# Optimization experiments

Measured on AMD Instinct MI355X. Metric: run time of the kernel, lower is better.

Reference implementation:

```python
import jax, jax.numpy as jnp
import numpy as np

B, C, N, K, OUT = 8, 128, 8192, 16, 128

def setup_inputs() -> dict:
    key = jax.random.key(0)
    k1, k2, k3, k4 = jax.random.split(key, 4)
    x = jax.random.normal(k1, (B, C, N), dtype=jnp.float32)
    idx = jax.random.randint(k2, (B * N * K,), 0, B * N, dtype=jnp.int64)
    W = jax.random.normal(k3, (OUT, C, 1), dtype=jnp.float32) * 0.05
    b = jax.random.normal(k4, (OUT,), dtype=jnp.float32) * 0.05
    return {"x": x, "idx": idx, "W": W, "b": b}

def reference(x, idx, W, b):
    Bs, Cs, Ns = x.shape
    k = idx.shape[0] // (Bs * Ns)
    # (B,C,N) -> (B*N, C) matching torch permute(0,2,1).reshape(-1,C)
    x_flat = jnp.transpose(x, (0, 2, 1)).reshape(-1, Cs)
    # gather k neighbors per point, then max over neighbor dim
    neighbors = x_flat[idx].reshape(Bs, Ns, k, Cs)  # (B,N,k,C)
    agg = neighbors.max(axis=2)                      # (B,N,C)
    # 1x1 conv == per-point linear: (B,N,C) x (O,C) -> (B,O,N)
    out = jnp.einsum('bnc,oc->bon', agg, W[:, :, 0]) + b[None, :, None]
    return jax.nn.relu(out)
```

## Files before the change

### kernel.cpp

```cpp
#include <hip/hip_runtime.h>
#include <stdint.h>

#define B_  8
#define C_  128
#define N_  8192
#define K_  16
#define O_  128

typedef __attribute__((ext_vector_type(8))) short short8;
typedef __attribute__((ext_vector_type(4))) float f32x4;

__device__ __forceinline__ unsigned short f2bf(float f) {
    union { float f; uint32_t u; } v; v.f = f;
    uint32_t u = v.u;
    return (unsigned short)((u + 0x7FFFu + ((u >> 16) & 1u)) >> 16);
}

__device__ __forceinline__ uint32_t fwdmap(uint32_t u) {
    uint32_t s  = u & 0x80008000u;
    uint32_t xm = s - (s >> 15) + 0x80008000u;
    return u ^ xm;
}
__device__ __forceinline__ uint32_t invmap(uint32_t v) {
    uint32_t s  = (~v) & 0x80008000u;
    uint32_t xm = s - (s >> 15) + 0x80008000u;
    return v ^ xm;
}
__device__ __forceinline__ uint32_t pkmax(uint32_t a, uint32_t b) {
    uint32_t d;
    asm("v_pk_max_u16 %0, %1, %2" : "=v"(d) : "v"(a), "v"(b));
    return d;
}
__device__ __forceinline__ uint4 pkmax4(uint4 a, uint4 b) {
    return make_uint4(pkmax(a.x, b.x), pkmax(a.y, b.y),
                      pkmax(a.z, b.z), pkmax(a.w, b.w));
}

__global__ __launch_bounds__(256) void k_transpose(const float* __restrict__ x,
                                                   unsigned short* __restrict__ xt) {
    __shared__ uint32_t lds[64 * 65];
    int t    = threadIdx.x;
    int lane = t & 63;
    int wv   = t >> 6;
    int blk  = blockIdx.x;
    int b    = blk >> 7;
    int n0   = (blk & 127) * 64;

    const float* xb = x + (size_t)b * C_ * N_ + n0 + lane;
    #pragma unroll
    for (int j = 0; j < 16; ++j) {
        int c2 = wv * 16 + j;
        float f0 = xb[(size_t)(2 * c2) * N_];
        float f1 = xb[(size_t)(2 * c2 + 1) * N_];
        uint32_t pk = (uint32_t)f2bf(f0) | ((uint32_t)f2bf(f1) << 16);
        lds[c2 * 65 + lane] = fwdmap(pk);
    }
    __syncthreads();

    int rl = lane >> 4;
    int ch = lane & 15;
    #pragma unroll
    for (int it = 0; it < 4; ++it) {
        int r = it * 16 + wv * 4 + rl;
        uint32_t u0 = lds[(ch * 4 + 0) * 65 + r];
        uint32_t u1 = lds[(ch * 4 + 1) * 65 + r];
        uint32_t u2 = lds[(ch * 4 + 2) * 65 + r];
        uint32_t u3 = lds[(ch * 4 + 3) * 65 + r];
        *(uint4*)(xt + ((size_t)(b * N_ + n0 + r)) * C_ + ch * 8) =
            make_uint4(u0, u1, u2, u3);
    }
}

__global__ __launch_bounds__(256, 4) void k_main(const unsigned short* __restrict__ xt,
                                                 const int* __restrict__ idx,
                                                 const float* __restrict__ Wp,
                                                 const float* __restrict__ bp,
                                                 float* __restrict__ out) {
    __shared__ __align__(16) unsigned short agg[64 * 136];
    __shared__ int idxs[64 * K_];

    int t    = threadIdx.x;
    int lane = t & 63;
    int wv   = t >> 6;
    int blk  = blockIdx.x;
    int b    = blk >> 7;
    int n0   = (blk & 127) * 64;
    size_t pbase = (size_t)b * N_ + n0;

    const int* ip = idx + pbase * K_;
    #pragma unroll
    for (int i = 0; i < 4; ++i) idxs[t + i * 256] = ip[t + i * 256];
    __syncthreads();

    int pt  = lane >> 4;
    int cch = lane & 15;
    #pragma unroll
    for (int i = 0; i < 4; ++i) {
        int p = wv * 16 + i * 4 + pt;
        const int* qq = &idxs[p * K_];
        uint4 d[16];
        #pragma unroll
        for (int k = 0; k < 16; ++k)
            d[k] = *(const uint4*)(xt + (size_t)qq[k] * C_ + cch * 8);
        #pragma unroll
        for (int s = 8; s >= 1; s >>= 1)
            #pragma unroll
            for (int k = 0; k < s; ++k)
                d[k] = pkmax4(d[k], d[k + s]);
        uint4 v = make_uint4(invmap(d[0].x), invmap(d[0].y),
                             invmap(d[0].z), invmap(d[0].w));
        *(uint4*)&agg[p * 136 + cch * 8] = v;
    }
    __syncthreads();

    int r16 = lane & 15;
    int h   = lane >> 4;
    int wo  = wv * 32;

    short8 af[2][4];
    #pragma unroll
    for (int ot2 = 0; ot2 < 2; ++ot2)
        #pragma unroll
        for (int kk = 0; kk < 4; ++kk) {
            const float* wr = Wp + (size_t)(wo + ot2 * 16 + r16) * C_ + kk * 32 + h * 8;
            float4 a0 = *(const float4*)wr;
            float4 a1 = *(const float4*)(wr + 4);
            short8 s;
            s[0] = (short)f2bf(a0.x); s[1] = (short)f2bf(a0.y);
            s[2] = (short)f2bf(a0.z); s[3] = (short)f2bf(a0.w);
            s[4] = (short)f2bf(a1.x); s[5] = (short)f2bf(a1.y);
            s[6] = (short)f2bf(a1.z); s[7] = (short)f2bf(a1.w);
            af[ot2][kk] = s;
        }
    float4 bb[2];
    bb[0] = *(const float4*)(bp + wo + h * 4);
    bb[1] = *(const float4*)(bp + wo + 16 + h * 4);

    const size_t ob = (size_t)b * O_ * N_ + n0;
    #pragma unroll
    for (int pt4 = 0; pt4 < 4; ++pt4) {
        short8 bfr[4];
        #pragma unroll
        for (int kk = 0; kk < 4; ++kk)
            bfr[kk] = *(const short8*)&agg[(pt4 * 16 + r16) * 136 + kk * 32 + h * 8];
        #pragma unroll
        for (int ot2 = 0; ot2 < 2; ++ot2) {
            f32x4 acc = {0.f, 0.f, 0.f, 0.f};
            #pragma unroll
            for (int kk = 0; kk < 4; ++kk)
                acc = __builtin_amdgcn_mfma_f32_16x16x32_bf16(af[ot2][kk], bfr[kk], acc, 0, 0, 0);
            int orow = wo + ot2 * 16 + h * 4;
            float* op = out + ob + (size_t)orow * N_ + pt4 * 16 + r16;
            float4 bv = bb[ot2];
            op[0]              = fmaxf(acc[0] + bv.x, 0.f);
            op[(size_t)N_]     = fmaxf(acc[1] + bv.y, 0.f);
            op[(size_t)2 * N_] = fmaxf(acc[2] + bv.z, 0.f);
            op[(size_t)3 * N_] = fmaxf(acc[3] + bv.w, 0.f);
        }
    }
}

extern "C" void kernel_launch(void* const* d_in, const int* in_sizes, int n_in,
                              void* d_out, int out_size, void* d_ws, size_t ws_size,
                              hipStream_t stream) {
    const float* x    = (const float*)d_in[0];
    const int*   idx  = (const int*)d_in[1];
    const float* W    = (const float*)d_in[2];
    const float* bias = (const float*)d_in[3];
    float* out = (float*)d_out;
    unsigned short* xt = (unsigned short*)d_ws;

    hipLaunchKernelGGL(k_transpose, dim3(1024), dim3(256), 0, stream, x, xt);
    hipLaunchKernelGGL(k_main,      dim3(1024), dim3(256), 0, stream, xt, idx, W, bias, out);
}
```

Measured before the change: 52.90 us.

## Split bf16 feature table into channel planes and halve gather tile size

The transposed bf16 feature table is now stored as four 32-channel planes instead of one 128-channel row per point. The gather-max kernel reads each plane with 8-byte loads and runs two 8-way max trees per plane. The main kernel now handles 32 points per block across 2048 blocks with a higher occupancy bound. A spare block in the transpose kernel pre-converts W to bf16 when the workspace is large enough. The aim is better cache locality for the random gathers and more parallelism, at the cost of smaller, less coalesced gather segments and more blocks.

```diff
diff --git a/kernel.cpp b/kernel.cpp
--- a/kernel.cpp
+++ b/kernel.cpp
@@ -6,6 +6,8 @@
 #define N_  8192
 #define K_  16
 #define O_  128
+#define TP  32
+#define PL  ((size_t)65536 * 32)
 
 typedef __attribute__((ext_vector_type(8))) short short8;
 typedef __attribute__((ext_vector_type(4))) float f32x4;
@@ -15,7 +17,6 @@
     uint32_t u = v.u;
     return (unsigned short)((u + 0x7FFFu + ((u >> 16) & 1u)) >> 16);
 }
-
 __device__ __forceinline__ uint32_t fwdmap(uint32_t u) {
     uint32_t s  = u & 0x80008000u;
     uint32_t xm = s - (s >> 15) + 0x80008000u;
@@ -31,18 +32,36 @@
     asm("v_pk_max_u16 %0, %1, %2" : "=v"(d) : "v"(a), "v"(b));
     return d;
 }
-__device__ __forceinline__ uint4 pkmax4(uint4 a, uint4 b) {
-    return make_uint4(pkmax(a.x, b.x), pkmax(a.y, b.y),
-                      pkmax(a.z, b.z), pkmax(a.w, b.w));
-}
-
+__device__ __forceinline__ uint2 pkmax2(uint2 a, uint2 b) {
+    return make_uint2(pkmax(a.x, b.x), pkmax(a.y, b.y));
+}
+__device__ __forceinline__ uint2 tree8(const uint2 d[8]) {
+    uint2 t0 = pkmax2(d[0], d[4]), t1 = pkmax2(d[1], d[5]);
+    uint2 t2 = pkmax2(d[2], d[6]), t3 = pkmax2(d[3], d[7]);
+    t0 = pkmax2(t0, t2); t1 = pkmax2(t1, t3);
+    return pkmax2(t0, t1);
+}
+
+template<bool PREW>
 __global__ __launch_bounds__(256) void k_transpose(const float* __restrict__ x,
-                                                   unsigned short* __restrict__ xt) {
-    __shared__ uint32_t lds[64 * 65];
+                                                   unsigned short* __restrict__ xt,
+                                                   const float* __restrict__ Wp,
+                                                   unsigned short* __restrict__ Wbf) {
+    int blk = blockIdx.x;
+    if (PREW && blk == 1024) {
+        int t = threadIdx.x;
+        #pragma unroll
+        for (int i = 0; i < 32; ++i) {
+            int e = t + i * 256;
+            float2 w2 = ((const float2*)Wp)[e];
+            ((uint32_t*)Wbf)[e] = (uint32_t)f2bf(w2.x) | ((uint32_t)f2bf(w2.y) << 16);
+        }
+        return;
+    }
+    __shared__ uint32_t lds[64 * 66];
     int t    = threadIdx.x;
     int lane = t & 63;
     int wv   = t >> 6;
-    int blk  = blockIdx.x;
     int b    = blk >> 7;
     int n0   = (blk & 127) * 64;
 
@@ -53,105 +72,109 @@
         float f0 = xb[(size_t)(2 * c2) * N_];
         float f1 = xb[(size_t)(2 * c2 + 1) * N_];
         uint32_t pk = (uint32_t)f2bf(f0) | ((uint32_t)f2bf(f1) << 16);
-        lds[c2 * 65 + lane] = fwdmap(pk);
+        lds[c2 * 66 + lane] = fwdmap(pk);
     }
     __syncthreads();
 
-    int rl = lane >> 4;
-    int ch = lane & 15;
-    #pragma unroll
-    for (int it = 0; it < 4; ++it) {
-        int r = it * 16 + wv * 4 + rl;
-        uint32_t u0 = lds[(ch * 4 + 0) * 65 + r];
-        uint32_t u1 = lds[(ch * 4 + 1) * 65 + r];
-        uint32_t u2 = lds[(ch * 4 + 2) * 65 + r];
-        uint32_t u3 = lds[(ch * 4 + 3) * 65 + r];
-        *(uint4*)(xt + ((size_t)(b * N_ + n0 + r)) * C_ + ch * 8) =
+    int rr = lane >> 2;
+    int ch = lane & 3;
+    size_t rowb = (size_t)(b * N_ + n0);
+    #pragma unroll
+    for (int pl = 0; pl < 4; ++pl) {
+        int r = wv * 16 + rr;
+        uint32_t u0 = lds[(pl * 16 + ch * 4 + 0) * 66 + r];
+        uint32_t u1 = lds[(pl * 16 + ch * 4 + 1) * 66 + r];
+        uint32_t u2 = lds[(pl * 16 + ch * 4 + 2) * 66 + r];
+        uint32_t u3 = lds[(pl * 16 + ch * 4 + 3) * 66 + r];
+        *(uint4*)(xt + (size_t)pl * PL + (rowb + r) * 32 + ch * 8) =
             make_uint4(u0, u1, u2, u3);
     }
 }
 
-__global__ __launch_bounds__(256, 4) void k_main(const unsigned short* __restrict__ xt,
+template<bool PREW>
+__global__ __launch_bounds__(256, 8) void k_main(const unsigned short* __restrict__ xt,
                                                  const int* __restrict__ idx,
                                                  const float* __restrict__ Wp,
+                                                 const unsigned short* __restrict__ Wbf,
                                                  const float* __restrict__ bp,
                                                  float* __restrict__ out) {
-    __shared__ __align__(16) unsigned short agg[64 * 136];
-    __shared__ int idxs[64 * K_];
+    __shared__ __align__(16) unsigned short agg[TP * 136];
+    __shared__ int idxs[TP * K_];
 
     int t    = threadIdx.x;
     int lane = t & 63;
     int wv   = t >> 6;
     int blk  = blockIdx.x;
-    int b    = blk >> 7;
-    int n0   = (blk & 127) * 64;
+    int b    = blk >> 8;
+    int n0   = (blk & 255) * TP;
     size_t pbase = (size_t)b * N_ + n0;
 
     const int* ip = idx + pbase * K_;
-    #pragma unroll
-    for (int i = 0; i < 4; ++i) idxs[t + i * 256] = ip[t + i * 256];
+    idxs[t]       = ip[t];
+    idxs[t + 256] = ip[t + 256];
     __syncthreads();
 
-    int pt  = lane >> 4;
-    int cch = lane & 15;
-    #pragma unroll
-    for (int i = 0; i < 4; ++i) {
-        int p = wv * 16 + i * 4 + pt;
-        const int* qq = &idxs[p * K_];
-        uint4 d[16];
-        #pragma unroll
-        for (int k = 0; k < 16; ++k)
-            d[k] = *(const uint4*)(xt + (size_t)qq[k] * C_ + cch * 8);
-        #pragma unroll
-        for (int s = 8; s >= 1; s >>= 1)
-            #pragma unroll
-            for (int k = 0; k < s; ++k)
-                d[k] = pkmax4(d[k], d[k + s]);
-        uint4 v = make_uint4(invmap(d[0].x), invmap(d[0].y),
-                             invmap(d[0].z), invmap(d[0].w));
-        *(uint4*)&agg[p * 136 + cch * 8] = v;
+    int pt  = lane >> 3;
+    int cch = lane & 7;
+    int p   = wv * 8 + pt;
+    const int* qq = &idxs[p * K_];
+    #pragma unroll
+    for (int pl = 0; pl < 4; ++pl) {
+        const unsigned short* base = xt + (size_t)pl * PL + cch * 4;
+        uint2 d[8];
+        #pragma unroll
+        for (int k = 0; k < 8; ++k)
+            d[k] = *(const uint2*)(base + (size_t)qq[k] * 32);
+        uint2 r0 = tree8(d);
+        #pragma unroll
+        for (int k = 0; k < 8; ++k)
+            d[k] = *(const uint2*)(base + (size_t)qq[k + 8] * 32);
+        uint2 r1 = tree8(d);
+        uint2 r  = pkmax2(r0, r1);
+        *(uint2*)&agg[p * 136 + pl * 32 + cch * 4] =
+            make_uint2(invmap(r.x), invmap(r.y));
     }
     __syncthreads();
 
     int r16 = lane & 15;
     int h   = lane >> 4;
     int wo  = wv * 32;
-
-    short8 af[2][4];
-    #pragma unroll
-    for (int ot2 = 0; ot2 < 2; ++ot2)
-        #pragma unroll
-        for (int kk = 0; kk < 4; ++kk) {
-            const float* wr = Wp + (size_t)(wo + ot2 * 16 + r16) * C_ + kk * 32 + h * 8;
-            float4 a0 = *(const float4*)wr;
-            float4 a1 = *(const float4*)(wr + 4);
-            short8 s;
-            s[0] = (short)f2bf(a0.x); s[1] = (short)f2bf(a0.y);
-            s[2] = (short)f2bf(a0.z); s[3] = (short)f2bf(a0.w);
-            s[4] = (short)f2bf(a1.x); s[5] = (short)f2bf(a1.y);
-            s[6] = (short)f2bf(a1.z); s[7] = (short)f2bf(a1.w);
-            af[ot2][kk] = s;
+    const size_t ob = (size_t)b * O_ * N_ + n0;
+
+    #pragma unroll
+    for (int ot2 = 0; ot2 < 2; ++ot2) {
+        short8 af[4];
+        if (PREW) {
+            #pragma unroll
+            for (int kk = 0; kk < 4; ++kk)
+                af[kk] = *(const short8*)(Wbf + (size_t)(wo + ot2 * 16 + r16) * C_ + kk * 32 + h * 8);
+        } else {
+            #pragma unroll
+            for (int kk = 0; kk < 4; ++kk) {
+                const float* wr = Wp + (size_t)(wo + ot2 * 16 + r16) * C_ + kk * 32 + h * 8;
+                float4 a0 = *(const float4*)wr;
+                float4 a1 = *(const float4*)(wr + 4);
+                short8 s;
+                s[0] = (short)f2bf(a0.x); s[1] = (short)f2bf(a0.y);
+                s[2] = (short)f2bf(a0.z); s[3] = (short)f2bf(a0.w);
+                s[4] = (short)f2bf(a1.x); s[5] = (short)f2bf(a1.y);
+                s[6] = (short)f2bf(a1.z); s[7] = (short)f2bf(a1.w);
+                af[kk] = s;
+            }
         }
-    float4 bb[2];
-    bb[0] = *(const float4*)(bp + wo + h * 4);
-    bb[1] = *(const float4*)(bp + wo + 16 + h * 4);
-
-    const size_t ob = (size_t)b * O_ * N_ + n0;
-    #pragma unroll
-    for (int pt4 = 0; pt4 < 4; ++pt4) {
-        short8 bfr[4];
-        #pragma unroll
-        for (int kk = 0; kk < 4; ++kk)
-            bfr[kk] = *(const short8*)&agg[(pt4 * 16 + r16) * 136 + kk * 32 + h * 8];
-        #pragma unroll
-        for (int ot2 = 0; ot2 < 2; ++ot2) {
+        float4 bv = *(const float4*)(bp + wo + ot2 * 16 + h * 4);
+        int orow = wo + ot2 * 16 + h * 4;
+        #pragma unroll
+        for (int pt4 = 0; pt4 < 2; ++pt4) {
+            short8 bfr[4];
+            #pragma unroll
+            for (int kk = 0; kk < 4; ++kk)
+                bfr[kk] = *(const short8*)&agg[(pt4 * 16 + r16) * 136 + kk * 32 + h * 8];
             f32x4 acc = {0.f, 0.f, 0.f, 0.f};
             #pragma unroll
             for (int kk = 0; kk < 4; ++kk)
-                acc = __builtin_amdgcn_mfma_f32_16x16x32_bf16(af[ot2][kk], bfr[kk], acc, 0, 0, 0);
-            int orow = wo + ot2 * 16 + h * 4;
+                acc = __builtin_amdgcn_mfma_f32_16x16x32_bf16(af[kk], bfr[kk], acc, 0, 0, 0);
             float* op = out + ob + (size_t)orow * N_ + pt4 * 16 + r16;
-            float4 bv = bb[ot2];
             op[0]              = fmaxf(acc[0] + bv.x, 0.f);
             op[(size_t)N_]     = fmaxf(acc[1] + bv.y, 0.f);
             op[(size_t)2 * N_] = fmaxf(acc[2] + bv.z, 0.f);
@@ -163,13 +186,23 @@
 extern "C" void kernel_launch(void* const* d_in, const int* in_sizes, int n_in,
                               void* d_out, int out_size, void* d_ws, size_t ws_size,
                               hipStream_t stream) {
+    (void)in_sizes; (void)n_in; (void)out_size;
     const float* x    = (const float*)d_in[0];
     const int*   idx  = (const int*)d_in[1];
     const float* W    = (const float*)d_in[2];
     const float* bias = (const float*)d_in[3];
     float* out = (float*)d_out;
-    unsigned short* xt = (unsigned short*)d_ws;
-
-    hipLaunchKernelGGL(k_transpose, dim3(1024), dim3(256), 0, stream, x, xt);
-    hipLaunchKernelGGL(k_main,      dim3(1024), dim3(256), 0, stream, xt, idx, W, bias, out);
-}
+
+    const size_t XTB = (size_t)4 * PL * 2;
+    unsigned short* xt  = (unsigned short*)d_ws;
+    unsigned short* wbf = (unsigned short*)((char*)d_ws + XTB);
+    bool prew = ws_size >= XTB + O_ * C_ * 2;
+
+    if (prew) {
+        hipLaunchKernelGGL(k_transpose<true>,  dim3(1025), dim3(256), 0, stream, x, xt, W, wbf);
+        hipLaunchKernelGGL(k_main<true>,       dim3(2048), dim3(256), 0, stream, xt, idx, W, wbf, bias, out);
+    } else {
+        hipLaunchKernelGGL(k_transpose<false>, dim3(1024), dim3(256), 0, stream, x, xt, W, wbf);
+        hipLaunchKernelGGL(k_main<false>,      dim3(2048), dim3(256), 0, stream, xt, idx, W, wbf, bias, out);
+    }
+}
```

Result: slower. 69.70 us (+31.7%).
